# Kernel tuning notes

Measured on AMD Instinct MI355X. Metric: run time of the kernel, lower is better.

The kernel has to match this reference:

```python
import jax, jax.numpy as jnp
import numpy as np


def setup_inputs() -> dict:
    key = jax.random.key(0)
    x = jax.random.normal(key, (4, 4096, 128), dtype=jnp.float32)
    return {"x": x}


def reference(x) -> jnp.ndarray:
    # Unnormalized bilinear self-attention with Q=K=V=x (no softmax).
    # scores[b,t,s] = sum_d x[b,t,d] x[b,s,d]; out[b,t,d] = sum_s scores[b,t,s] x[b,s,d]
    scores = jnp.einsum('btd,bsd->bts', x, x)  # [B,T,T]
    out = jnp.einsum('bts,bsd->btd', scores, x)  # [B,T,D]
    return out
```

## Files before the change

### kernel.cpp

```cpp
#include <hip/hip_runtime.h>

#define BATCH 4
#define T 4096
#define D 128
#define CHUNKS 64
#define ROWS1 64
#define ROWS2 64
#define ST1 72
#define S2 136

typedef __attribute__((ext_vector_type(4))) float f32x4;
typedef __attribute__((ext_vector_type(8))) short bf16x8;

__device__ __forceinline__ unsigned short f2b(float f) {
    unsigned u = __builtin_bit_cast(unsigned, f);
    u += 0x7FFFu + ((u >> 16) & 1u);
    return (unsigned short)(u >> 16);
}
__device__ __forceinline__ float b2f(unsigned short h) {
    return __builtin_bit_cast(float, (unsigned)h << 16);
}

__global__ __launch_bounds__(256) void k_gram(const float* __restrict__ x,
                                              unsigned short* __restrict__ part) {
    __shared__ unsigned short XT[D * ST1];
    const int blk = blockIdx.x;
    const int b = blk >> 6, chunk = blk & 63;
    const float* xp = x + ((size_t)b * T + (size_t)chunk * ROWS1) * D;
    const int tid = threadIdx.x;

    #pragma unroll
    for (int pass = 0; pass < 8; pass++) {
        const int slot = (tid >> 6) + 4 * pass;
        const int dd = 2 * (tid & 7) + 16 * (slot & 7);
        const int tpg = ((tid >> 3) & 7) + 8 * (slot >> 3);
        const int t = 2 * tpg;
        float2 f0 = *(const float2*)(xp + (size_t)t * D + dd);
        float2 f1 = *(const float2*)(xp + (size_t)(t + 1) * D + dd);
        unsigned u0 = (unsigned)f2b(f0.x) | ((unsigned)f2b(f1.x) << 16);
        unsigned u1 = (unsigned)f2b(f0.y) | ((unsigned)f2b(f1.y) << 16);
        *(unsigned*)(XT + dd * ST1 + 2 * tpg) = u0;
        *(unsigned*)(XT + (dd + 1) * ST1 + 2 * tpg) = u1;
    }
    __syncthreads();

    const int lane = tid & 63, w = tid >> 6;
    const int m = lane & 15, q = lane >> 4;
    const int m0 = w * 32;

    f32x4 acc[2][8];
    #pragma unroll
    for (int mi = 0; mi < 2; mi++)
        #pragma unroll
        for (int ni = 0; ni < 8; ni++) acc[mi][ni] = (f32x4){0.f, 0.f, 0.f, 0.f};

    #pragma unroll
    for (int s = 0; s < 2; s++) {
        bf16x8 av[2], bv[8];
        #pragma unroll
        for (int mi = 0; mi < 2; mi++)
            av[mi] = *(const bf16x8*)(XT + (m0 + mi * 16 + m) * ST1 + q * 8 + s * 32);
        #pragma unroll
        for (int ni = 0; ni < 8; ni++)
            bv[ni] = *(const bf16x8*)(XT + (ni * 16 + m) * ST1 + q * 8 + s * 32);
        #pragma unroll
        for (int mi = 0; mi < 2; mi++)
            #pragma unroll
            for (int ni = 0; ni < 8; ni++)
                acc[mi][ni] = __builtin_amdgcn_mfma_f32_16x16x32_bf16(av[mi], bv[ni], acc[mi][ni], 0, 0, 0);
    }

    unsigned short* pp = part + (size_t)blk * (D * D);
    #pragma unroll
    for (int mi = 0; mi < 2; mi++)
        #pragma unroll
        for (int ni = 0; ni < 8; ni++) {
            const int row0 = m0 + mi * 16 + q * 4;
            const int col = ni * 16 + m;
            #pragma unroll
            for (int r = 0; r < 4; r++)
                pp[(size_t)(row0 + r) * D + col] = f2b(acc[mi][ni][r]);
        }
}

__global__ __launch_bounds__(256) void k_reduce_g(const unsigned short* __restrict__ part,
                                                  unsigned short* __restrict__ g) {
    const int o = blockIdx.x * 256 + threadIdx.x;
    const int b = o >> 14;
    const int e = o & 16383;
    const unsigned short* p = part + ((size_t)b * CHUNKS) * (D * D) + e;
    float s[8];
    #pragma unroll
    for (int i = 0; i < 8; i++) s[i] = 0.f;
    for (int c = 0; c < CHUNKS; c += 8) {
        #pragma unroll
        for (int i = 0; i < 8; i++)
            s[i] += b2f(p[(size_t)(c + i) * (D * D)]);
    }
    float sum = ((s[0] + s[1]) + (s[2] + s[3])) + ((s[4] + s[5]) + (s[6] + s[7]));
    g[o] = f2b(sum);
}

__global__ __launch_bounds__(256) void k_xg_mfma(const float* __restrict__ x,
                                                 const unsigned short* __restrict__ g,
                                                 float* __restrict__ out) {
    __shared__ unsigned short Xs[ROWS2 * S2];
    __shared__ unsigned short Gs[D * S2];
    const int blk = blockIdx.x;
    const int b = blk >> 6, chunk = blk & 63;
    const float* xp = x + ((size_t)b * T + (size_t)chunk * ROWS2) * D;
    const unsigned short* gp = g + (size_t)b * (D * D);
    const int tid = threadIdx.x;

    {
        const int dg = tid & 31, tr = tid >> 5;
        #pragma unroll
        for (int ii = 0; ii < 8; ii++) {
            const int t = tr + ii * 8;
            float4 v = ((const float4*)(xp + t * D))[dg];
            ushort4 pk;
            pk.x = f2b(v.x); pk.y = f2b(v.y); pk.z = f2b(v.z); pk.w = f2b(v.w);
            *(ushort4*)(Xs + t * S2 + dg * 4) = pk;
        }
    }
    {
        const int f4 = tid & 15, r = tid >> 4;
        #pragma unroll
        for (int ii = 0; ii < 8; ii++) {
            const int row = r + ii * 16;
            uint4 gv = ((const uint4*)(gp + row * D))[f4];
            *(uint4*)(Gs + row * S2 + f4 * 8) = gv;
        }
    }
    __syncthreads();

    const int lane = tid & 63, w = tid >> 6;
    const int m = lane & 15, q = lane >> 4;

    f32x4 acc[8];
    #pragma unroll
    for (int ni = 0; ni < 8; ni++) acc[ni] = (f32x4){0.f, 0.f, 0.f, 0.f};

    const unsigned short* arow = Xs + (w * 16 + m) * S2 + q * 8;
    const unsigned short* brow = Gs + m * S2 + q * 8;

    #pragma unroll
    for (int s = 0; s < 4; s++) {
        bf16x8 a = *(const bf16x8*)(arow + s * 32);
        #pragma unroll
        for (int ni = 0; ni < 8; ni++) {
            bf16x8 bb = *(const bf16x8*)(brow + ni * 16 * S2 + s * 32);
            acc[ni] = __builtin_amdgcn_mfma_f32_16x16x32_bf16(a, bb, acc[ni], 0, 0, 0);
        }
    }

    float* op = out + ((size_t)b * T + (size_t)chunk * ROWS2) * D;
    const int row0 = w * 16 + q * 4;
    #pragma unroll
    for (int ni = 0; ni < 8; ni++)
        #pragma unroll
        for (int r = 0; r < 4; r++)
            op[(row0 + r) * D + ni * 16 + m] = acc[ni][r];
}

extern "C" void kernel_launch(void* const* d_in, const int* in_sizes, int n_in,
                              void* d_out, int out_size, void* d_ws, size_t ws_size,
                              hipStream_t stream) {
    const float* x = (const float*)d_in[0];
    float* out = (float*)d_out;

    const size_t part_elems = (size_t)BATCH * CHUNKS * D * D;
    unsigned short* part = (unsigned short*)d_ws;
    unsigned short* g = part + part_elems;

    k_gram<<<BATCH * CHUNKS, 256, 0, stream>>>(x, part);
    k_reduce_g<<<BATCH * D * D / 256, 256, 0, stream>>>(part, g);
    k_xg_mfma<<<BATCH * 64, 256, 0, stream>>>(x, g, out);
}
```

Measured before the change: 68.87 us.

## Fuse gram, reduce and XG kernels into one persistent kernel with grid barriers

Merges the three launches into a single 256-block kernel that separates the phases with atomic-counter grid barriers, and adds a memset to reset the counters. Each thread now writes its partial-Gram accumulators contiguously as vector stores in a permuted layout, and the reduction phase un-permutes the result when writing g. The aim is to remove inter-kernel launch gaps and to make the partial writes coalesced. In exchange it relies on all 256 blocks being co-resident for the spin barriers to make progress, adds a memset call, and pays for barrier spinning.

```diff
diff --git a/kernel.cpp b/kernel.cpp
--- a/kernel.cpp
+++ b/kernel.cpp
@@ -4,10 +4,10 @@
 #define T 4096
 #define D 128
 #define CHUNKS 64
-#define ROWS1 64
-#define ROWS2 64
+#define ROWS 64
 #define ST1 72
 #define S2 136
+#define NBLK (BATCH * CHUNKS)
 
 typedef __attribute__((ext_vector_type(4))) float f32x4;
 typedef __attribute__((ext_vector_type(8))) short bf16x8;
@@ -21,146 +21,162 @@
     return __builtin_bit_cast(float, (unsigned)h << 16);
 }
 
-__global__ __launch_bounds__(256) void k_gram(const float* __restrict__ x,
-                                              unsigned short* __restrict__ part) {
-    __shared__ unsigned short XT[D * ST1];
+__device__ __forceinline__ void grid_barrier(unsigned* ctr, int tid) {
+    __syncthreads();
+    __threadfence();
+    if (tid == 0) {
+        atomicAdd(ctr, 1u);
+        while (atomicAdd(ctr, 0u) < NBLK)
+            __builtin_amdgcn_s_sleep(1);
+    }
+    __syncthreads();
+    __threadfence();
+}
+
+__global__ __launch_bounds__(256) void k_fused(const float* __restrict__ x,
+                                               unsigned short* __restrict__ part,
+                                               unsigned short* __restrict__ g,
+                                               float* __restrict__ out,
+                                               unsigned* __restrict__ bar) {
+    __shared__ unsigned short smem[(ROWS + D) * S2];
+    const int tid = threadIdx.x;
     const int blk = blockIdx.x;
     const int b = blk >> 6, chunk = blk & 63;
-    const float* xp = x + ((size_t)b * T + (size_t)chunk * ROWS1) * D;
-    const int tid = threadIdx.x;
-
-    #pragma unroll
-    for (int pass = 0; pass < 8; pass++) {
-        const int slot = (tid >> 6) + 4 * pass;
-        const int dd = 2 * (tid & 7) + 16 * (slot & 7);
-        const int tpg = ((tid >> 3) & 7) + 8 * (slot >> 3);
-        const int t = 2 * tpg;
-        float2 f0 = *(const float2*)(xp + (size_t)t * D + dd);
-        float2 f1 = *(const float2*)(xp + (size_t)(t + 1) * D + dd);
-        unsigned u0 = (unsigned)f2b(f0.x) | ((unsigned)f2b(f1.x) << 16);
-        unsigned u1 = (unsigned)f2b(f0.y) | ((unsigned)f2b(f1.y) << 16);
-        *(unsigned*)(XT + dd * ST1 + 2 * tpg) = u0;
-        *(unsigned*)(XT + (dd + 1) * ST1 + 2 * tpg) = u1;
-    }
-    __syncthreads();
-
+    const float* xp = x + ((size_t)b * T + (size_t)chunk * ROWS) * D;
     const int lane = tid & 63, w = tid >> 6;
     const int m = lane & 15, q = lane >> 4;
-    const int m0 = w * 32;
 
-    f32x4 acc[2][8];
-    #pragma unroll
-    for (int mi = 0; mi < 2; mi++)
+    {
+        unsigned short* XT = smem;
         #pragma unroll
-        for (int ni = 0; ni < 8; ni++) acc[mi][ni] = (f32x4){0.f, 0.f, 0.f, 0.f};
+        for (int pass = 0; pass < 8; pass++) {
+            const int slot = (tid >> 6) + 4 * pass;
+            const int dd = 2 * (tid & 7) + 16 * (slot & 7);
+            const int tpg = ((tid >> 3) & 7) + 8 * (slot >> 3);
+            const int t = 2 * tpg;
+            float2 f0 = *(const float2*)(xp + (size_t)t * D + dd);
+            float2 f1 = *(const float2*)(xp + (size_t)(t + 1) * D + dd);
+            unsigned u0 = (unsigned)f2b(f0.x) | ((unsigned)f2b(f1.x) << 16);
+            unsigned u1 = (unsigned)f2b(f0.y) | ((unsigned)f2b(f1.y) << 16);
+            *(unsigned*)(XT + dd * ST1 + 2 * tpg) = u0;
+            *(unsigned*)(XT + (dd + 1) * ST1 + 2 * tpg) = u1;
+        }
+        __syncthreads();
 
-    #pragma unroll
-    for (int s = 0; s < 2; s++) {
-        bf16x8 av[2], bv[8];
-        #pragma unroll
-        for (int mi = 0; mi < 2; mi++)
-            av[mi] = *(const bf16x8*)(XT + (m0 + mi * 16 + m) * ST1 + q * 8 + s * 32);
-        #pragma unroll
-        for (int ni = 0; ni < 8; ni++)
-            bv[ni] = *(const bf16x8*)(XT + (ni * 16 + m) * ST1 + q * 8 + s * 32);
+        const int m0 = w * 32;
+        f32x4 acc[2][8];
         #pragma unroll
         for (int mi = 0; mi < 2; mi++)
             #pragma unroll
+            for (int ni = 0; ni < 8; ni++) acc[mi][ni] = (f32x4){0.f, 0.f, 0.f, 0.f};
+
+        #pragma unroll
+        for (int s = 0; s < 2; s++) {
+            bf16x8 av[2], bv[8];
+            #pragma unroll
+            for (int mi = 0; mi < 2; mi++)
+                av[mi] = *(const bf16x8*)(XT + (m0 + mi * 16 + m) * ST1 + q * 8 + s * 32);
+            #pragma unroll
             for (int ni = 0; ni < 8; ni++)
-                acc[mi][ni] = __builtin_amdgcn_mfma_f32_16x16x32_bf16(av[mi], bv[ni], acc[mi][ni], 0, 0, 0);
-    }
+                bv[ni] = *(const bf16x8*)(XT + (ni * 16 + m) * ST1 + q * 8 + s * 32);
+            #pragma unroll
+            for (int mi = 0; mi < 2; mi++)
+                #pragma unroll
+                for (int ni = 0; ni < 8; ni++)
+                    acc[mi][ni] = __builtin_amdgcn_mfma_f32_16x16x32_bf16(av[mi], bv[ni], acc[mi][ni], 0, 0, 0);
+        }
 
-    unsigned short* pp = part + (size_t)blk * (D * D);
-    #pragma unroll
-    for (int mi = 0; mi < 2; mi++)
+        unsigned short* pp = part + (size_t)blk * (D * D) + (size_t)tid * 64;
         #pragma unroll
-        for (int ni = 0; ni < 8; ni++) {
-            const int row0 = m0 + mi * 16 + q * 4;
-            const int col = ni * 16 + m;
-            #pragma unroll
-            for (int r = 0; r < 4; r++)
-                pp[(size_t)(row0 + r) * D + col] = f2b(acc[mi][ni][r]);
-        }
-}
-
-__global__ __launch_bounds__(256) void k_reduce_g(const unsigned short* __restrict__ part,
-                                                  unsigned short* __restrict__ g) {
-    const int o = blockIdx.x * 256 + threadIdx.x;
-    const int b = o >> 14;
-    const int e = o & 16383;
-    const unsigned short* p = part + ((size_t)b * CHUNKS) * (D * D) + e;
-    float s[8];
-    #pragma unroll
-    for (int i = 0; i < 8; i++) s[i] = 0.f;
-    for (int c = 0; c < CHUNKS; c += 8) {
-        #pragma unroll
-        for (int i = 0; i < 8; i++)
-            s[i] += b2f(p[(size_t)(c + i) * (D * D)]);
-    }
-    float sum = ((s[0] + s[1]) + (s[2] + s[3])) + ((s[4] + s[5]) + (s[6] + s[7]));
-    g[o] = f2b(sum);
-}
-
-__global__ __launch_bounds__(256) void k_xg_mfma(const float* __restrict__ x,
-                                                 const unsigned short* __restrict__ g,
-                                                 float* __restrict__ out) {
-    __shared__ unsigned short Xs[ROWS2 * S2];
-    __shared__ unsigned short Gs[D * S2];
-    const int blk = blockIdx.x;
-    const int b = blk >> 6, chunk = blk & 63;
-    const float* xp = x + ((size_t)b * T + (size_t)chunk * ROWS2) * D;
-    const unsigned short* gp = g + (size_t)b * (D * D);
-    const int tid = threadIdx.x;
-
-    {
-        const int dg = tid & 31, tr = tid >> 5;
-        #pragma unroll
-        for (int ii = 0; ii < 8; ii++) {
-            const int t = tr + ii * 8;
-            float4 v = ((const float4*)(xp + t * D))[dg];
-            ushort4 pk;
-            pk.x = f2b(v.x); pk.y = f2b(v.y); pk.z = f2b(v.z); pk.w = f2b(v.w);
-            *(ushort4*)(Xs + t * S2 + dg * 4) = pk;
-        }
-    }
-    {
-        const int f4 = tid & 15, r = tid >> 4;
-        #pragma unroll
-        for (int ii = 0; ii < 8; ii++) {
-            const int row = r + ii * 16;
-            uint4 gv = ((const uint4*)(gp + row * D))[f4];
-            *(uint4*)(Gs + row * S2 + f4 * 8) = gv;
-        }
-    }
-    __syncthreads();
-
-    const int lane = tid & 63, w = tid >> 6;
-    const int m = lane & 15, q = lane >> 4;
-
-    f32x4 acc[8];
-    #pragma unroll
-    for (int ni = 0; ni < 8; ni++) acc[ni] = (f32x4){0.f, 0.f, 0.f, 0.f};
-
-    const unsigned short* arow = Xs + (w * 16 + m) * S2 + q * 8;
-    const unsigned short* brow = Gs + m * S2 + q * 8;
-
-    #pragma unroll
-    for (int s = 0; s < 4; s++) {
-        bf16x8 a = *(const bf16x8*)(arow + s * 32);
-        #pragma unroll
-        for (int ni = 0; ni < 8; ni++) {
-            bf16x8 bb = *(const bf16x8*)(brow + ni * 16 * S2 + s * 32);
-            acc[ni] = __builtin_amdgcn_mfma_f32_16x16x32_bf16(a, bb, acc[ni], 0, 0, 0);
+        for (int j = 0; j < 8; j++) {
+            const int mi = j >> 2, nj = (j & 3) * 2;
+            ushort4 lo, hi;
+            lo.x = f2b(acc[mi][nj][0]);     lo.y = f2b(acc[mi][nj][1]);
+            lo.z = f2b(acc[mi][nj][2]);     lo.w = f2b(acc[mi][nj][3]);
+            hi.x = f2b(acc[mi][nj + 1][0]); hi.y = f2b(acc[mi][nj + 1][1]);
+            hi.z = f2b(acc[mi][nj + 1][2]); hi.w = f2b(acc[mi][nj + 1][3]);
+            *(ushort4*)(pp + j * 8) = lo;
+            *(ushort4*)(pp + j * 8 + 4) = hi;
         }
     }
 
-    float* op = out + ((size_t)b * T + (size_t)chunk * ROWS2) * D;
-    const int row0 = w * 16 + q * 4;
-    #pragma unroll
-    for (int ni = 0; ni < 8; ni++)
+    grid_barrier(bar, tid);
+
+    {
+        const int o = blk * 256 + tid;
+        const int ob = o >> 14, e = o & 16383;
+        const unsigned short* p = part + ((size_t)ob * CHUNKS) * (D * D) + e;
+        float s[8];
         #pragma unroll
-        for (int r = 0; r < 4; r++)
-            op[(row0 + r) * D + ni * 16 + m] = acc[ni][r];
+        for (int i = 0; i < 8; i++) s[i] = 0.f;
+        for (int c = 0; c < CHUNKS; c += 8) {
+            #pragma unroll
+            for (int i = 0; i < 8; i++)
+                s[i] += b2f(p[(size_t)(c + i) * (D * D)]);
+        }
+        float sum = ((s[0] + s[1]) + (s[2] + s[3])) + ((s[4] + s[5]) + (s[6] + s[7]));
+        const int tg = e >> 6, sub = e & 63;
+        const int gw = tg >> 6, gl = tg & 63, gm = gl & 15, gq = gl >> 4;
+        const int mi = sub >> 5, ni = (sub >> 2) & 7, r = sub & 3;
+        const int row = gw * 32 + mi * 16 + gq * 4 + r;
+        const int col = ni * 16 + gm;
+        g[(size_t)ob * (D * D) + row * D + col] = f2b(sum);
+    }
+
+    grid_barrier(bar + 1, tid);
+
+    {
+        unsigned short* Xs = smem;
+        unsigned short* Gs = smem + ROWS * S2;
+        const unsigned short* gp = g + (size_t)b * (D * D);
+
+        {
+            const int dg = tid & 31, tr = tid >> 5;
+            #pragma unroll
+            for (int ii = 0; ii < 8; ii++) {
+                const int t = tr + ii * 8;
+                float4 v = ((const float4*)(xp + t * D))[dg];
+                ushort4 pk;
+                pk.x = f2b(v.x); pk.y = f2b(v.y); pk.z = f2b(v.z); pk.w = f2b(v.w);
+                *(ushort4*)(Xs + t * S2 + dg * 4) = pk;
+            }
+        }
+        {
+            const int f4 = tid & 15, r = tid >> 4;
+            #pragma unroll
+            for (int ii = 0; ii < 8; ii++) {
+                const int row = r + ii * 16;
+                uint4 gv = ((const uint4*)(gp + row * D))[f4];
+                *(uint4*)(Gs + row * S2 + f4 * 8) = gv;
+            }
+        }
+        __syncthreads();
+
+        f32x4 acc[8];
+        #pragma unroll
+        for (int ni = 0; ni < 8; ni++) acc[ni] = (f32x4){0.f, 0.f, 0.f, 0.f};
+
+        const unsigned short* arow = Xs + (w * 16 + m) * S2 + q * 8;
+        const unsigned short* brow = Gs + m * S2 + q * 8;
+
+        #pragma unroll
+        for (int s = 0; s < 4; s++) {
+            bf16x8 a = *(const bf16x8*)(arow + s * 32);
+            #pragma unroll
+            for (int ni = 0; ni < 8; ni++) {
+                bf16x8 bb = *(const bf16x8*)(brow + ni * 16 * S2 + s * 32);
+                acc[ni] = __builtin_amdgcn_mfma_f32_16x16x32_bf16(a, bb, acc[ni], 0, 0, 0);
+            }
+        }
+
+        float* op = out + ((size_t)b * T + (size_t)chunk * ROWS) * D;
+        const int row0 = w * 16 + q * 4;
+        #pragma unroll
+        for (int ni = 0; ni < 8; ni++)
+            #pragma unroll
+            for (int r = 0; r < 4; r++)
+                op[(row0 + r) * D + ni * 16 + m] = acc[ni][r];
+    }
 }
 
 extern "C" void kernel_launch(void* const* d_in, const int* in_sizes, int n_in,
@@ -169,11 +185,12 @@
     const float* x = (const float*)d_in[0];
     float* out = (float*)d_out;
 
-    const size_t part_elems = (size_t)BATCH * CHUNKS * D * D;
+    const size_t part_elems = (size_t)NBLK * D * D;
+    const size_t g_elems = (size_t)BATCH * D * D;
     unsigned short* part = (unsigned short*)d_ws;
     unsigned short* g = part + part_elems;
+    unsigned* bar = (unsigned*)(g + g_elems);
 
-    k_gram<<<BATCH * CHUNKS, 256, 0, stream>>>(x, part);
-    k_reduce_g<<<BATCH * D * D / 256, 256, 0, stream>>>(part, g);
-    k_xg_mfma<<<BATCH * 64, 256, 0, stream>>>(x, g, out);
+    hipMemsetAsync(bar, 0, 2 * sizeof(unsigned), stream);
+    k_fused<<<NBLK, 256, 0, stream>>>(x, part, g, out, bar);
 }
```

New measurement: 182.2 us. 165% more time.

## Accumulate Gram over larger slabs and fuse partial reduction into output GEMM

Applied to the files above, without the earlier changes.

The Gram kernel now has each block loop over eight 64-row tiles of a 512-row slab and accumulate in registers, so only 8 partial Gram matrices per batch are written instead of 64. The separate reduction kernel is removed, and each output block sums the 8 bf16 partials while loading G into shared memory. This cuts one launch and most of the partial-matrix traffic. In exchange the Gram kernel launches only 32 blocks, which leaves most CUs idle, and every output block repeats the same partial reduction.

```diff
diff --git a/kernel.cpp b/kernel.cpp
--- a/kernel.cpp
+++ b/kernel.cpp
@@ -3,9 +3,9 @@
 #define BATCH 4
 #define T 4096
 #define D 128
-#define CHUNKS 64
-#define ROWS1 64
-#define ROWS2 64
+#define SLABS 8
+#define SROWS 512
+#define ROWS 64
 #define ST1 72
 #define S2 136
 
@@ -17,33 +17,20 @@
     u += 0x7FFFu + ((u >> 16) & 1u);
     return (unsigned short)(u >> 16);
 }
-__device__ __forceinline__ float b2f(unsigned short h) {
-    return __builtin_bit_cast(float, (unsigned)h << 16);
+__device__ __forceinline__ float b2f_lo(unsigned u) {
+    return __builtin_bit_cast(float, u << 16);
+}
+__device__ __forceinline__ float b2f_hi(unsigned u) {
+    return __builtin_bit_cast(float, u & 0xFFFF0000u);
 }
 
 __global__ __launch_bounds__(256) void k_gram(const float* __restrict__ x,
                                               unsigned short* __restrict__ part) {
     __shared__ unsigned short XT[D * ST1];
     const int blk = blockIdx.x;
-    const int b = blk >> 6, chunk = blk & 63;
-    const float* xp = x + ((size_t)b * T + (size_t)chunk * ROWS1) * D;
+    const int b = blk >> 3, slab = blk & 7;
+    const float* xp = x + ((size_t)b * T + (size_t)slab * SROWS) * D;
     const int tid = threadIdx.x;
-
-    #pragma unroll
-    for (int pass = 0; pass < 8; pass++) {
-        const int slot = (tid >> 6) + 4 * pass;
-        const int dd = 2 * (tid & 7) + 16 * (slot & 7);
-        const int tpg = ((tid >> 3) & 7) + 8 * (slot >> 3);
-        const int t = 2 * tpg;
-        float2 f0 = *(const float2*)(xp + (size_t)t * D + dd);
-        float2 f1 = *(const float2*)(xp + (size_t)(t + 1) * D + dd);
-        unsigned u0 = (unsigned)f2b(f0.x) | ((unsigned)f2b(f1.x) << 16);
-        unsigned u1 = (unsigned)f2b(f0.y) | ((unsigned)f2b(f1.y) << 16);
-        *(unsigned*)(XT + dd * ST1 + 2 * tpg) = u0;
-        *(unsigned*)(XT + (dd + 1) * ST1 + 2 * tpg) = u1;
-    }
-    __syncthreads();
-
     const int lane = tid & 63, w = tid >> 6;
     const int m = lane & 15, q = lane >> 4;
     const int m0 = w * 32;
@@ -54,20 +41,39 @@
         #pragma unroll
         for (int ni = 0; ni < 8; ni++) acc[mi][ni] = (f32x4){0.f, 0.f, 0.f, 0.f};
 
-    #pragma unroll
-    for (int s = 0; s < 2; s++) {
-        bf16x8 av[2], bv[8];
+    for (int kt = 0; kt < SROWS / 64; kt++) {
+        const float* xk = xp + (size_t)kt * 64 * D;
+        if (kt) __syncthreads();
         #pragma unroll
-        for (int mi = 0; mi < 2; mi++)
-            av[mi] = *(const bf16x8*)(XT + (m0 + mi * 16 + m) * ST1 + q * 8 + s * 32);
+        for (int pass = 0; pass < 8; pass++) {
+            const int slot = (tid >> 6) + 4 * pass;
+            const int dd = 2 * (tid & 7) + 16 * (slot & 7);
+            const int tpg = ((tid >> 3) & 7) + 8 * (slot >> 3);
+            const int t = 2 * tpg;
+            float2 f0 = *(const float2*)(xk + (size_t)t * D + dd);
+            float2 f1 = *(const float2*)(xk + (size_t)(t + 1) * D + dd);
+            unsigned u0 = (unsigned)f2b(f0.x) | ((unsigned)f2b(f1.x) << 16);
+            unsigned u1 = (unsigned)f2b(f0.y) | ((unsigned)f2b(f1.y) << 16);
+            *(unsigned*)(XT + dd * ST1 + 2 * tpg) = u0;
+            *(unsigned*)(XT + (dd + 1) * ST1 + 2 * tpg) = u1;
+        }
+        __syncthreads();
+
         #pragma unroll
-        for (int ni = 0; ni < 8; ni++)
-            bv[ni] = *(const bf16x8*)(XT + (ni * 16 + m) * ST1 + q * 8 + s * 32);
-        #pragma unroll
-        for (int mi = 0; mi < 2; mi++)
+        for (int s = 0; s < 2; s++) {
+            bf16x8 av[2], bv[8];
+            #pragma unroll
+            for (int mi = 0; mi < 2; mi++)
+                av[mi] = *(const bf16x8*)(XT + (m0 + mi * 16 + m) * ST1 + q * 8 + s * 32);
             #pragma unroll
             for (int ni = 0; ni < 8; ni++)
-                acc[mi][ni] = __builtin_amdgcn_mfma_f32_16x16x32_bf16(av[mi], bv[ni], acc[mi][ni], 0, 0, 0);
+                bv[ni] = *(const bf16x8*)(XT + (ni * 16 + m) * ST1 + q * 8 + s * 32);
+            #pragma unroll
+            for (int mi = 0; mi < 2; mi++)
+                #pragma unroll
+                for (int ni = 0; ni < 8; ni++)
+                    acc[mi][ni] = __builtin_amdgcn_mfma_f32_16x16x32_bf16(av[mi], bv[ni], acc[mi][ni], 0, 0, 0);
+        }
     }
 
     unsigned short* pp = part + (size_t)blk * (D * D);
@@ -83,33 +89,15 @@
         }
 }
 
-__global__ __launch_bounds__(256) void k_reduce_g(const unsigned short* __restrict__ part,
-                                                  unsigned short* __restrict__ g) {
-    const int o = blockIdx.x * 256 + threadIdx.x;
-    const int b = o >> 14;
-    const int e = o & 16383;
-    const unsigned short* p = part + ((size_t)b * CHUNKS) * (D * D) + e;
-    float s[8];
-    #pragma unroll
-    for (int i = 0; i < 8; i++) s[i] = 0.f;
-    for (int c = 0; c < CHUNKS; c += 8) {
-        #pragma unroll
-        for (int i = 0; i < 8; i++)
-            s[i] += b2f(p[(size_t)(c + i) * (D * D)]);
-    }
-    float sum = ((s[0] + s[1]) + (s[2] + s[3])) + ((s[4] + s[5]) + (s[6] + s[7]));
-    g[o] = f2b(sum);
-}
-
-__global__ __launch_bounds__(256) void k_xg_mfma(const float* __restrict__ x,
-                                                 const unsigned short* __restrict__ g,
-                                                 float* __restrict__ out) {
-    __shared__ unsigned short Xs[ROWS2 * S2];
+__global__ __launch_bounds__(256) void k_xg_r(const float* __restrict__ x,
+                                              const unsigned short* __restrict__ part,
+                                              float* __restrict__ out) {
+    __shared__ unsigned short Xs[ROWS * S2];
     __shared__ unsigned short Gs[D * S2];
     const int blk = blockIdx.x;
     const int b = blk >> 6, chunk = blk & 63;
-    const float* xp = x + ((size_t)b * T + (size_t)chunk * ROWS2) * D;
-    const unsigned short* gp = g + (size_t)b * (D * D);
+    const float* xp = x + ((size_t)b * T + (size_t)chunk * ROWS) * D;
+    const unsigned short* pb = part + (size_t)b * SLABS * (D * D);
     const int tid = threadIdx.x;
 
     {
@@ -128,8 +116,23 @@
         #pragma unroll
         for (int ii = 0; ii < 8; ii++) {
             const int row = r + ii * 16;
-            uint4 gv = ((const uint4*)(gp + row * D))[f4];
-            *(uint4*)(Gs + row * S2 + f4 * 8) = gv;
+            const unsigned short* base = pb + (size_t)row * D + f4 * 8;
+            float s[8];
+            #pragma unroll
+            for (int i = 0; i < 8; i++) s[i] = 0.f;
+            #pragma unroll
+            for (int c = 0; c < SLABS; c++) {
+                uint4 gv = *(const uint4*)(base + (size_t)c * (D * D));
+                s[0] += b2f_lo(gv.x); s[1] += b2f_hi(gv.x);
+                s[2] += b2f_lo(gv.y); s[3] += b2f_hi(gv.y);
+                s[4] += b2f_lo(gv.z); s[5] += b2f_hi(gv.z);
+                s[6] += b2f_lo(gv.w); s[7] += b2f_hi(gv.w);
+            }
+            ushort4 lo4, hi4;
+            lo4.x = f2b(s[0]); lo4.y = f2b(s[1]); lo4.z = f2b(s[2]); lo4.w = f2b(s[3]);
+            hi4.x = f2b(s[4]); hi4.y = f2b(s[5]); hi4.z = f2b(s[6]); hi4.w = f2b(s[7]);
+            *(ushort4*)(Gs + row * S2 + f4 * 8) = lo4;
+            *(ushort4*)(Gs + row * S2 + f4 * 8 + 4) = hi4;
         }
     }
     __syncthreads();
@@ -154,7 +157,7 @@
         }
     }
 
-    float* op = out + ((size_t)b * T + (size_t)chunk * ROWS2) * D;
+    float* op = out + ((size_t)b * T + (size_t)chunk * ROWS) * D;
     const int row0 = w * 16 + q * 4;
     #pragma unroll
     for (int ni = 0; ni < 8; ni++)
@@ -169,11 +172,8 @@
     const float* x = (const float*)d_in[0];
     float* out = (float*)d_out;
 
-    const size_t part_elems = (size_t)BATCH * CHUNKS * D * D;
     unsigned short* part = (unsigned short*)d_ws;
-    unsigned short* g = part + part_elems;
 
-    k_gram<<<BATCH * CHUNKS, 256, 0, stream>>>(x, part);
-    k_reduce_g<<<BATCH * D * D / 256, 256, 0, stream>>>(part, g);
-    k_xg_mfma<<<BATCH * 64, 256, 0, stream>>>(x, g, out);
+    k_gram<<<BATCH * SLABS, 256, 0, stream>>>(x, part);
+    k_xg_r<<<BATCH * 64, 256, 0, stream>>>(x, part, out);
 }
```

Measured after the change: 89.67 us. 1.3x slower.
